# Performance work log

Hardware: AMD Instinct MI355X
Metric: run time of the kernel (lower is better)

## Reference

```python
import jax, jax.numpy as jnp
import numpy as np

DIM = 768
NUM_HEADS = 12
HEAD_DIM = DIM // NUM_HEADS
SCALE = HEAD_DIM ** -0.5


def setup_inputs() -> dict:
    key = jax.random.key(0)
    k1, k2, k3, k4 = jax.random.split(key, 4)
    B, N = 2, 4096
    x = jax.random.normal(k1, (B, N, DIM), dtype=jnp.float32)
    # qkv: nn.Linear(dim, 3*dim, bias=False)
    W_qkv = jax.random.normal(k2, (DIM, 3 * DIM), dtype=jnp.float32) * (DIM ** -0.5)
    # proj: nn.Linear(dim, dim) with bias
    W_proj = jax.random.normal(k3, (DIM, DIM), dtype=jnp.float32) * (DIM ** -0.5)
    b_proj = jax.random.normal(k4, (DIM,), dtype=jnp.float32) * 0.02
    return {"x": x, "W_qkv": W_qkv, "W_proj": W_proj, "b_proj": b_proj}


def reference(x, W_qkv, W_proj, b_proj):
    B, N, C = x.shape
    qkv = x @ W_qkv  # [B, N, 3C]
    qkv = qkv.reshape(B, N, 3, NUM_HEADS, HEAD_DIM)
    q = qkv[:, :, 0].transpose(0, 2, 1, 3)  # [B, H, N, D]
    k = qkv[:, :, 1].transpose(0, 2, 1, 3)
    v = qkv[:, :, 2].transpose(0, 2, 1, 3)
    attn = jnp.einsum('bhnd,bhmd->bhnm', q, k) * SCALE  # [B, H, N, N]
    attn = jax.nn.softmax(attn, axis=-1)
    out = jnp.einsum('bhnm,bhmd->bhnd', attn, v)  # [B, H, N, D]
    out = out.transpose(0, 2, 1, 3).reshape(B, N, C)
    return out @ W_proj + b_proj
```

## Files before the change

### kernel.cpp

```cpp
#include <hip/hip_runtime.h>
#include <stdint.h>

#define NBATCH 2
#define SEQ    4096
#define CDIM   768
#define NHEADS 12
#define HDIM   64
#define MTOK   (NBATCH*SEQ)
#define TC3    (3*CDIM)
#define QSCALE (0.125f * 1.4426950408889634f)
#define SMAX 12.0f

typedef unsigned short u16;
typedef __attribute__((ext_vector_type(8))) short bh8;
typedef __attribute__((ext_vector_type(4))) float f32x4;
typedef __attribute__((ext_vector_type(16))) float f32x16;
typedef __attribute__((ext_vector_type(4))) unsigned short us4;
typedef __attribute__((ext_vector_type(8))) unsigned short us8;

__device__ __forceinline__ u16 f2bf(float f) {
  union { float f; uint32_t u; } v; v.f = f;
  return (u16)((v.u + 0x7FFFu + ((v.u >> 16) & 1u)) >> 16);
}

__device__ __forceinline__ uint32_t cvt_pk_bf16(float a, float b) {
  uint32_t r;
  asm("v_cvt_pk_bf16_f32 %0, %1, %2" : "=v"(r) : "v"(a), "v"(b));
  return r;
}

#define GL_LDS16(src, dst) \
  __builtin_amdgcn_global_load_lds((const __attribute__((address_space(1))) void*)(src), \
                                   (__attribute__((address_space(3))) void*)(dst), 16, 0, 0)

__global__ void cast_x_kernel(const float* __restrict__ in, u16* __restrict__ out, int n4) {
  int i = blockIdx.x * blockDim.x + threadIdx.x;
  if (i >= n4) return;
  float4 v = ((const float4*)in)[i];
  us4 o;
  o[0] = f2bf(v.x); o[1] = f2bf(v.y); o[2] = f2bf(v.z); o[3] = f2bf(v.w);
  ((us4*)out)[i] = o;
}

__global__ void transpose_cast_kernel(const float* __restrict__ in, u16* __restrict__ out,
                                      int R, int C) {
  __shared__ float t[32][33];
  int c0 = blockIdx.x * 32, r0 = blockIdx.y * 32;
  int tx = threadIdx.x, ty = threadIdx.y;
#pragma unroll
  for (int i = 0; i < 4; ++i)
    t[ty + 8 * i][tx] = in[(r0 + ty + 8 * i) * C + c0 + tx];
  __syncthreads();
#pragma unroll
  for (int i = 0; i < 4; ++i)
    out[(c0 + ty + 8 * i) * R + r0 + tx] = f2bf(t[tx][ty + 8 * i]);
}

__global__ __launch_bounds__(256) void gemm_qkv_kernel(
    const u16* __restrict__ A, const u16* __restrict__ Bt,
    u16* __restrict__ Qs, u16* __restrict__ Kb, u16* __restrict__ Vt) {
  __shared__ __align__(16) u16 As[128 * 32];
  __shared__ __align__(16) u16 Bs[128 * 32];
  int blk = blockIdx.x;
  int bm = blk / 18, bn = blk % 18;
  int m0 = bm * 128, n0 = bn * 128;
  int tid = threadIdx.x;
  int wv = tid >> 6, ln = tid & 63;
  int wr = wv >> 1, wc = wv & 1;

  f32x4 acc[4][4];
#pragma unroll
  for (int i = 0; i < 4; ++i)
#pragma unroll
    for (int j = 0; j < 4; ++j) acc[i][j] = (f32x4){0.f, 0.f, 0.f, 0.f};

  const char* Ab = (const char*)(A + m0 * CDIM);
  const char* Bb = (const char*)(Bt + n0 * CDIM);

  for (int kt = 0; kt < CDIM / 32; ++kt) {
#pragma unroll
    for (int i = 0; i < 2; ++i) {
      int idx = i * 256 + tid;
      int r = idx >> 2, c = idx & 3;
      int cs = c ^ ((r >> 1) & 3);
      GL_LDS16(Ab + r * (CDIM * 2) + kt * 64 + cs * 16, (char*)As + idx * 16);
      GL_LDS16(Bb + r * (CDIM * 2) + kt * 64 + cs * 16, (char*)Bs + idx * 16);
    }
    __syncthreads();

    bh8 af[4];
#pragma unroll
    for (int mi = 0; mi < 4; ++mi) {
      int r = 64 * wr + 16 * mi + (ln & 15);
      int cs = (ln >> 4) ^ ((r >> 1) & 3);
      af[mi] = *(const bh8*)((const char*)As + r * 64 + cs * 16);
    }
#pragma unroll
    for (int nj = 0; nj < 4; ++nj) {
      int r = 64 * wc + 16 * nj + (ln & 15);
      int cs = (ln >> 4) ^ ((r >> 1) & 3);
      bh8 bf = *(const bh8*)((const char*)Bs + r * 64 + cs * 16);
#pragma unroll
      for (int mi = 0; mi < 4; ++mi)
        acc[mi][nj] = __builtin_amdgcn_mfma_f32_16x16x32_bf16(af[mi], bf, acc[mi][nj], 0, 0, 0);
    }
    __syncthreads();
  }

  int b = m0 >> 12;
#pragma unroll
  for (int nj = 0; nj < 4; ++nj) {
    int nb = n0 + 64 * wc + 16 * nj;
    int which = nb / CDIM;
    int rem = nb % CDIM;
    int h = rem / 64;
    int d = (rem % 64) + (ln & 15);
#pragma unroll
    for (int mi = 0; mi < 4; ++mi) {
      int t0 = (m0 & 4095) + 64 * wr + 16 * mi + ((ln >> 4) << 2);
      f32x4 v = acc[mi][nj];
      if (which == 0) {
#pragma unroll
        for (int q = 0; q < 4; ++q)
          Qs[((b * 12 + h) * 4096 + t0 + q) * 64 + d] = f2bf(v[q] * QSCALE);
      } else if (which == 1) {
#pragma unroll
        for (int q = 0; q < 4; ++q)
          Kb[((b * 12 + h) * 4096 + t0 + q) * 64 + d] = f2bf(v[q]);
      } else {
        us4 o;
#pragma unroll
        for (int q = 0; q < 4; ++q) o[q] = f2bf(v[q]);
        *(us4*)(Vt + ((b * 12 + h) * 64 + d) * 4096 + t0) = o;
      }
    }
  }
}

__device__ __forceinline__ void softmax_pack(
    const f32x16& s, float& lsum, bh8& pf_lo, bh8& pf_hi) {
  float p[16];
#pragma unroll
  for (int e = 0; e < 16; ++e) { p[e] = __builtin_amdgcn_exp2f(s[e]); lsum += p[e]; }
  unsigned int W[8];
#pragma unroll
  for (int g = 0; g < 4; ++g) {
    W[2 * g]     = cvt_pk_bf16(p[4 * g],     p[4 * g + 1]);
    W[2 * g + 1] = cvt_pk_bf16(p[4 * g + 2], p[4 * g + 3]);
  }
  unsigned int a0 = W[0], a1 = W[2], b0 = W[1], b1 = W[3];
  asm("v_permlane32_swap_b32 %0, %1" : "+v"(a0), "+v"(a1));
  asm("v_permlane32_swap_b32 %0, %1" : "+v"(b0), "+v"(b1));
  unsigned int c0 = W[4], c1 = W[6], d0 = W[5], d1 = W[7];
  asm("v_permlane32_swap_b32 %0, %1" : "+v"(c0), "+v"(c1));
  asm("v_permlane32_swap_b32 %0, %1" : "+v"(d0), "+v"(d1));
  union { unsigned int u[4]; bh8 v; } u0, u1;
  u0.u[0] = a0; u0.u[1] = b0; u0.u[2] = a1; u0.u[3] = b1;
  u1.u[0] = c0; u1.u[1] = d0; u1.u[2] = c1; u1.u[3] = d1;
  pf_lo = u0.v; pf_hi = u1.v;
}

__device__ __forceinline__ void attn_half(
    const char* kb, const char* vb, const bh8* qf0, const bh8* qf1,
    f32x16* od, float& ls0, float& ls1, int kblk,
    int q31, int h, int x7) {
  const char* krow = kb + (kblk * 32 + q31) * 128;
  bh8 kf[4];
#pragma unroll
  for (int ks = 0; ks < 4; ++ks)
    kf[ks] = *(const bh8*)(krow + ((2 * ks + h) ^ x7) * 16);

  f32x16 s0, s1;
#pragma unroll
  for (int e = 0; e < 16; ++e) { s0[e] = -SMAX; s1[e] = -SMAX; }
  __builtin_amdgcn_s_setprio(1);
#pragma unroll
  for (int ks = 0; ks < 4; ++ks) {
    s0 = __builtin_amdgcn_mfma_f32_32x32x16_bf16(kf[ks], qf0[ks], s0, 0, 0, 0);
    s1 = __builtin_amdgcn_mfma_f32_32x32x16_bf16(kf[ks], qf1[ks], s1, 0, 0, 0);
  }
  __builtin_amdgcn_s_setprio(0);

  bh8 p0[2], p1[2];
  softmax_pack(s0, ls0, p0[0], p0[1]);
  softmax_pack(s1, ls1, p1[0], p1[1]);

  __builtin_amdgcn_s_setprio(1);
#pragma unroll
  for (int mm = 0; mm < 2; ++mm) {
    int cs = ((2 * (2 * kblk + mm) + h) ^ x7) * 16;
    bh8 v0 = *(const bh8*)(vb + q31 * 128 + cs);
    od[0] = __builtin_amdgcn_mfma_f32_32x32x16_bf16(v0, p0[mm], od[0], 0, 0, 0);
    od[1] = __builtin_amdgcn_mfma_f32_32x32x16_bf16(v0, p1[mm], od[1], 0, 0, 0);
    bh8 v1 = *(const bh8*)(vb + (32 + q31) * 128 + cs);
    od[2] = __builtin_amdgcn_mfma_f32_32x32x16_bf16(v1, p0[mm], od[2], 0, 0, 0);
    od[3] = __builtin_amdgcn_mfma_f32_32x32x16_bf16(v1, p1[mm], od[3], 0, 0, 0);
  }
  __builtin_amdgcn_s_setprio(0);
}

__global__ __launch_bounds__(256, 2) void attn_kernel(
    const u16* __restrict__ Qs, const u16* __restrict__ Kb,
    const u16* __restrict__ Vt,
    float* __restrict__ Op0, float* __restrict__ Op1, float* __restrict__ Lp) {
  __shared__ __align__(16) u16 Ks[2 * 64 * 64];
  __shared__ __align__(16) u16 Vs[2 * 64 * 64];
  int blk = blockIdx.x;
  int xcd = blk & 7, ii = blk >> 3;
  int bh = xcd + 8 * (ii >> 5);
  int rem = ii & 31;
  int h2 = rem >> 4;
  int qt = rem & 15;
  int tid = threadIdx.x, wv = tid >> 6, ln = tid & 63;
  int q31 = ln & 31, h = ln >> 5, x7 = ln & 7;

  const u16* qbase = Qs + (bh * 4096 + qt * 256 + wv * 64 + q31) * 64;
  bh8 qf0[4], qf1[4];
#pragma unroll
  for (int ks = 0; ks < 4; ++ks) {
    qf0[ks] = *(const bh8*)(qbase + 16 * ks + 8 * h);
    qf1[ks] = *(const bh8*)(qbase + 32 * 64 + 16 * ks + 8 * h);
  }

  f32x16 od[4];
#pragma unroll
  for (int i = 0; i < 4; ++i)
#pragma unroll
    for (int e = 0; e < 16; ++e) od[i][e] = 0.f;
  float ls0 = 0.f, ls1 = 0.f;

  const char* Kt0 = (const char*)(Kb + bh * 4096 * 64) + h2 * 2048 * 128;
  const char* Vt0 = (const char*)(Vt + bh * 64 * 4096) + h2 * 4096;

  int r0 = tid >> 3, c0 = tid & 7, cs0 = (c0 ^ (r0 & 7)) * 16;
  const char* ksrcA = Kt0 + r0 * 128 + cs0;
  const char* ksrcB = Kt0 + (r0 + 32) * 128 + cs0;
  const char* vsrcA = Vt0 + r0 * 8192 + cs0;
  const char* vsrcB = Vt0 + (r0 + 32) * 8192 + cs0;
  char* kd = (char*)Ks + tid * 16;
  char* vd = (char*)Vs + tid * 16;

  GL_LDS16(ksrcA, kd); GL_LDS16(ksrcB, kd + 4096);
  GL_LDS16(vsrcA, vd); GL_LDS16(vsrcB, vd + 4096);
  __syncthreads();

  const char* kb0 = (const char*)Ks; const char* kb1 = kb0 + 8192;
  const char* vb0 = (const char*)Vs; const char* vb1 = vb0 + 8192;

  for (int t = 0; t < 16; ++t) {
    GL_LDS16(ksrcA + (2 * t + 1) * 8192, kd + 8192);
    GL_LDS16(ksrcB + (2 * t + 1) * 8192, kd + 12288);
    GL_LDS16(vsrcA + (2 * t + 1) * 128, vd + 8192);
    GL_LDS16(vsrcB + (2 * t + 1) * 128, vd + 12288);
    attn_half(kb0, vb0, qf0, qf1, od, ls0, ls1, 0, q31, h, x7);
    __builtin_amdgcn_sched_barrier(0);
    attn_half(kb0, vb0, qf0, qf1, od, ls0, ls1, 1, q31, h, x7);
    __syncthreads();
    if (t < 15) {
      GL_LDS16(ksrcA + (2 * t + 2) * 8192, kd);
      GL_LDS16(ksrcB + (2 * t + 2) * 8192, kd + 4096);
      GL_LDS16(vsrcA + (2 * t + 2) * 128, vd);
      GL_LDS16(vsrcB + (2 * t + 2) * 128, vd + 4096);
    }
    attn_half(kb1, vb1, qf0, qf1, od, ls0, ls1, 0, q31, h, x7);
    __builtin_amdgcn_sched_barrier(0);
    attn_half(kb1, vb1, qf0, qf1, od, ls0, ls1, 1, q31, h, x7);
    __syncthreads();
  }

  float l0 = ls0 + __shfl_xor(ls0, 32);
  float l1 = ls1 + __shfl_xor(ls1, 32);

  int b = bh / 12, hd = bh % 12;
  int tok0 = qt * 256 + wv * 64 + q31;
  float* Op = h2 ? Op1 : Op0;
  float* ob0 = Op + (size_t)(b * 4096 + tok0) * 768 + hd * 64;
  float* ob1 = ob0 + 32 * 768;
#pragma unroll
  for (int db = 0; db < 2; ++db)
#pragma unroll
    for (int g = 0; g < 4; ++g) {
      float4 w0, w1;
      w0.x = od[2 * db][4 * g + 0]; w0.y = od[2 * db][4 * g + 1];
      w0.z = od[2 * db][4 * g + 2]; w0.w = od[2 * db][4 * g + 3];
      w1.x = od[2 * db + 1][4 * g + 0]; w1.y = od[2 * db + 1][4 * g + 1];
      w1.z = od[2 * db + 1][4 * g + 2]; w1.w = od[2 * db + 1][4 * g + 3];
      *(float4*)(ob0 + 32 * db + 8 * g + 4 * h) = w0;
      *(float4*)(ob1 + 32 * db + 8 * g + 4 * h) = w1;
    }
  if (h == 0) {
    Lp[h2 * (24 * 4096) + bh * 4096 + tok0] = l0;
    Lp[h2 * (24 * 4096) + bh * 4096 + tok0 + 32] = l1;
  }
}

__global__ __launch_bounds__(256) void combine_kernel(
    const float* __restrict__ Op0, const float* __restrict__ Op1,
    const float* __restrict__ Lp, u16* __restrict__ attn) {
  int idx = blockIdx.x * 256 + threadIdx.x;
  int i8 = idx * 8;
  int row = i8 / 768;
  int c = i8 - row * 768;
  int hd = c >> 6;
  int b = row >> 12, n = row & 4095;
  int li = (b * 12 + hd) * 4096 + n;
  float inv = 1.0f / (Lp[li] + Lp[24 * 4096 + li]);
  float4 a0 = *(const float4*)(Op0 + i8);
  float4 a1 = *(const float4*)(Op0 + i8 + 4);
  float4 b0 = *(const float4*)(Op1 + i8);
  float4 b1 = *(const float4*)(Op1 + i8 + 4);
  us8 w;
  w[0] = f2bf((a0.x + b0.x) * inv); w[1] = f2bf((a0.y + b0.y) * inv);
  w[2] = f2bf((a0.z + b0.z) * inv); w[3] = f2bf((a0.w + b0.w) * inv);
  w[4] = f2bf((a1.x + b1.x) * inv); w[5] = f2bf((a1.y + b1.y) * inv);
  w[6] = f2bf((a1.z + b1.z) * inv); w[7] = f2bf((a1.w + b1.w) * inv);
  *(us8*)(attn + i8) = w;
}

__global__ __launch_bounds__(256) void gemm_proj_kernel(
    const u16* __restrict__ A, const u16* __restrict__ Bt,
    const float* __restrict__ bias, float* __restrict__ out) {
  __shared__ __align__(16) u16 As[128 * 32];
  __shared__ __align__(16) u16 Bs[128 * 32];
  int blk = blockIdx.x;
  int bm = blk / 6, bn = blk % 6;
  int m0 = bm * 128, n0 = bn * 128;
  int tid = threadIdx.x;
  int wv = tid >> 6, ln = tid & 63;
  int wr = wv >> 1, wc = wv & 1;

  f32x4 acc[4][4];
#pragma unroll
  for (int i = 0; i < 4; ++i)
#pragma unroll
    for (int j = 0; j < 4; ++j) acc[i][j] = (f32x4){0.f, 0.f, 0.f, 0.f};

  const char* Ab = (const char*)(A + m0 * CDIM);
  const char* Bb = (const char*)(Bt + n0 * CDIM);

  for (int kt = 0; kt < CDIM / 32; ++kt) {
#pragma unroll
    for (int i = 0; i < 2; ++i) {
      int idx = i * 256 + tid;
      int r = idx >> 2, c = idx & 3;
      int cs = c ^ ((r >> 1) & 3);
      GL_LDS16(Ab + r * (CDIM * 2) + kt * 64 + cs * 16, (char*)As + idx * 16);
      GL_LDS16(Bb + r * (CDIM * 2) + kt * 64 + cs * 16, (char*)Bs + idx * 16);
    }
    __syncthreads();

    bh8 af[4];
#pragma unroll
    for (int mi = 0; mi < 4; ++mi) {
      int r = 64 * wr + 16 * mi + (ln & 15);
      int cs = (ln >> 4) ^ ((r >> 1) & 3);
      af[mi] = *(const bh8*)((const char*)As + r * 64 + cs * 16);
    }
#pragma unroll
    for (int nj = 0; nj < 4; ++nj) {
      int r = 64 * wc + 16 * nj + (ln & 15);
      int cs = (ln >> 4) ^ ((r >> 1) & 3);
      bh8 bf = *(const bh8*)((const char*)Bs + r * 64 + cs * 16);
#pragma unroll
      for (int mi = 0; mi < 4; ++mi)
        acc[mi][nj] = __builtin_amdgcn_mfma_f32_16x16x32_bf16(af[mi], bf, acc[mi][nj], 0, 0, 0);
    }
    __syncthreads();
  }

#pragma unroll
  for (int nj = 0; nj < 4; ++nj) {
    int col = n0 + 64 * wc + 16 * nj + (ln & 15);
    float bv = bias[col];
#pragma unroll
    for (int mi = 0; mi < 4; ++mi) {
      int row = m0 + 64 * wr + 16 * mi + ((ln >> 4) << 2);
#pragma unroll
      for (int q = 0; q < 4; ++q)
        out[(row + q) * CDIM + col] = acc[mi][nj][q] + bv;
    }
  }
}

extern "C" void kernel_launch(void* const* d_in, const int* in_sizes, int n_in,
                              void* d_out, int out_size, void* d_ws, size_t ws_size,
                              hipStream_t stream) {
  const float* x     = (const float*)d_in[0];
  const float* Wqkv  = (const float*)d_in[1];
  const float* Wproj = (const float*)d_in[2];
  const float* bias  = (const float*)d_in[3];
  float* out = (float*)d_out;

  u16* xb   = (u16*)d_ws;
  u16* Wqt  = xb + MTOK * CDIM;
  u16* Wpt  = Wqt + TC3 * CDIM;
  u16* Qs   = Wpt + CDIM * CDIM;
  u16* Kb   = Qs + 24 * 4096 * 64;
  u16* Vt   = Kb + 24 * 4096 * 64;
  u16* attn = Vt + 24 * 64 * 4096;
  float* Op1 = (float*)(attn + MTOK * CDIM);
  float* Lp  = Op1 + MTOK * CDIM;
  float* Op0 = out;

  cast_x_kernel<<<6144, 256, 0, stream>>>(x, xb, (MTOK * CDIM) / 4);
  transpose_cast_kernel<<<dim3(TC3 / 32, CDIM / 32), dim3(32, 8), 0, stream>>>(Wqkv, Wqt, CDIM, TC3);
  transpose_cast_kernel<<<dim3(CDIM / 32, CDIM / 32), dim3(32, 8), 0, stream>>>(Wproj, Wpt, CDIM, CDIM);
  gemm_qkv_kernel<<<(MTOK / 128) * (TC3 / 128), 256, 0, stream>>>(xb, Wqt, Qs, Kb, Vt);
  attn_kernel<<<768, 256, 0, stream>>>(Qs, Kb, Vt, Op0, Op1, Lp);
  combine_kernel<<<(MTOK * CDIM) / (256 * 8), 256, 0, stream>>>(Op0, Op1, Lp, attn);
  gemm_proj_kernel<<<(MTOK / 128) * (CDIM / 128), 256, 0, stream>>>(attn, Wpt, bias, out);
}
```

Measured before the change: 208.4 us.

## Restructure K/V double-buffer with partial vmcnt waits for deeper prefetch

Result: slower. 218.6 us (+4.9%).

```diff
diff --git a/kernel.cpp b/kernel.cpp
--- a/kernel.cpp
+++ b/kernel.cpp
@@ -240,33 +240,38 @@
   char* kd = (char*)Ks + tid * 16;
   char* vd = (char*)Vs + tid * 16;
 
-  GL_LDS16(ksrcA, kd); GL_LDS16(ksrcB, kd + 4096);
-  GL_LDS16(vsrcA, vd); GL_LDS16(vsrcB, vd + 4096);
-  __syncthreads();
-
-  const char* kb0 = (const char*)Ks; const char* kb1 = kb0 + 8192;
-  const char* vb0 = (const char*)Vs; const char* vb1 = vb0 + 8192;
-
-  for (int t = 0; t < 16; ++t) {
-    GL_LDS16(ksrcA + (2 * t + 1) * 8192, kd + 8192);
-    GL_LDS16(ksrcB + (2 * t + 1) * 8192, kd + 12288);
-    GL_LDS16(vsrcA + (2 * t + 1) * 128, vd + 8192);
-    GL_LDS16(vsrcB + (2 * t + 1) * 128, vd + 12288);
-    attn_half(kb0, vb0, qf0, qf1, od, ls0, ls1, 0, q31, h, x7);
+#define STAGE_T(tile, buf) do {                                  \
+    GL_LDS16(ksrcA + (tile) * 8192, kd + (buf) * 8192);          \
+    GL_LDS16(ksrcB + (tile) * 8192, kd + (buf) * 8192 + 4096);   \
+    GL_LDS16(vsrcA + (tile) * 128,  vd + (buf) * 8192);          \
+    GL_LDS16(vsrcB + (tile) * 128,  vd + (buf) * 8192 + 4096);   \
+  } while (0)
+
+  STAGE_T(0, 0);
+  STAGE_T(1, 1);
+
+  for (int t = 0; t < 31; ++t) {
+    int cur = t & 1;
+    asm volatile("s_waitcnt vmcnt(4)" ::: "memory");
+    __builtin_amdgcn_s_barrier();
+    const char* kb = (const char*)Ks + cur * 8192;
+    const char* vb = (const char*)Vs + cur * 8192;
+    attn_half(kb, vb, qf0, qf1, od, ls0, ls1, 0, q31, h, x7);
     __builtin_amdgcn_sched_barrier(0);
-    attn_half(kb0, vb0, qf0, qf1, od, ls0, ls1, 1, q31, h, x7);
-    __syncthreads();
-    if (t < 15) {
-      GL_LDS16(ksrcA + (2 * t + 2) * 8192, kd);
-      GL_LDS16(ksrcB + (2 * t + 2) * 8192, kd + 4096);
-      GL_LDS16(vsrcA + (2 * t + 2) * 128, vd);
-      GL_LDS16(vsrcB + (2 * t + 2) * 128, vd + 4096);
-    }
-    attn_half(kb1, vb1, qf0, qf1, od, ls0, ls1, 0, q31, h, x7);
+    attn_half(kb, vb, qf0, qf1, od, ls0, ls1, 1, q31, h, x7);
+    __builtin_amdgcn_s_barrier();
+    if (t + 2 < 32) STAGE_T(t + 2, cur);
+  }
+  asm volatile("s_waitcnt vmcnt(0)" ::: "memory");
+  __builtin_amdgcn_s_barrier();
+  {
+    const char* kb = (const char*)Ks + 8192;
+    const char* vb = (const char*)Vs + 8192;
+    attn_half(kb, vb, qf0, qf1, od, ls0, ls1, 0, q31, h, x7);
     __builtin_amdgcn_sched_barrier(0);
-    attn_half(kb1, vb1, qf0, qf1, od, ls0, ls1, 1, q31, h, x7);
-    __syncthreads();
-  }
+    attn_half(kb, vb, qf0, qf1, od, ls0, ls1, 1, q31, h, x7);
+  }
+#undef STAGE_T
 
   float l0 = ls0 + __shfl_xor(ls0, 32);
   float l1 = ls1 + __shfl_xor(ls1, 32);
```
